# Performance work log

Hardware: AMD Instinct MI355X
Metric: run time of the kernel (lower is better)

The kernel has to match this reference:

```python
import jax, jax.numpy as jnp
import numpy as np

N_NODES = 100000


def gcn_conv(x, src, dst, W, b, n_nodes):
    # PyG GCNConv with self-loops already appended to (src, dst):
    # out_i = sum_{(j->i)} deg_j^{-1/2} deg_i^{-1/2} (x_j @ W) + b
    h = x @ W  # [N, out]
    deg = jnp.zeros((n_nodes,), dtype=x.dtype).at[dst].add(1.0)
    dinv = jnp.where(deg > 0, deg ** -0.5, 0.0)
    norm = dinv[src] * dinv[dst]  # [E']
    msg = h[src] * norm[:, None]  # gather + scale
    out = jax.ops.segment_sum(msg, dst, num_segments=n_nodes)
    return out + b


def setup_inputs() -> dict:
    key = jax.random.key(0)
    ks = jax.random.split(key, 12)
    N, E = N_NODES, 1600000
    C_IN, C_HID, C_OUT = 128, 128, 64
    x = jax.random.normal(ks[0], (N, C_IN), dtype=jnp.float32)
    edge_index = jax.random.randint(ks[1], (2, E), 0, N, dtype=jnp.int64)

    def lin(k, fan_in, fan_out):
        s = 1.0 / np.sqrt(fan_in)
        return jax.random.uniform(k, (fan_in, fan_out), minval=-s, maxval=s, dtype=jnp.float32)

    return {
        "x": x,
        "edge_index": edge_index,
        "W0": lin(ks[2], C_IN, C_HID), "b0": jnp.zeros((C_HID,), jnp.float32),
        "W1": lin(ks[3], C_HID, C_HID), "b1": jnp.zeros((C_HID,), jnp.float32),
        "W2": lin(ks[4], C_HID, C_OUT), "b2": jnp.zeros((C_OUT,), jnp.float32),
        "mlp_w1": lin(ks[5], C_OUT, 64),
        "mlp_b1": jax.random.uniform(ks[6], (64,), minval=-1/8, maxval=1/8, dtype=jnp.float32),
        "mlp_w2": lin(ks[7], 64, 2),
        "mlp_b2": jax.random.uniform(ks[8], (2,), minval=-1/8, maxval=1/8, dtype=jnp.float32),
    }


def reference(x, edge_index, W0, b0, W1, b1, W2, b2, mlp_w1, mlp_b1, mlp_w2, mlp_b2):
    N = x.shape[0]
    src0, dst0 = edge_index[0], edge_index[1]
    loop = jnp.arange(N, dtype=edge_index.dtype)
    src = jnp.concatenate([src0, loop])  # self-loops appended
    dst = jnp.concatenate([dst0, loop])

    h = jax.nn.relu(gcn_conv(x, src, dst, W0, b0, N))
    h = jax.nn.relu(gcn_conv(h, src, dst, W1, b1, N))
    h = gcn_conv(h, src, dst, W2, b2, N)  # [N, out]

    # edge feature = mean of endpoint node features (original edges only)
    ef = (h[src0] + h[dst0]) * 0.5  # [E, out]
    y = jax.nn.relu(ef @ mlp_w1 + mlp_b1) @ mlp_w2 + mlp_b2  # [E, 2]
    return y
```

## Files before the change

### kernel.cpp

```cpp
#include <hip/hip_runtime.h>


__device__ __forceinline__ int edge_at(const int* __restrict__ ei, long long idx, int is32) {
    return is32 ? ei[idx] : ei[2 * idx];
}

__device__ __forceinline__ unsigned short f2bf(float f) {
    unsigned int u = __float_as_uint(f);
    u += 0x7FFFu + ((u >> 16) & 1u);
    return (unsigned short)(u >> 16);
}
__device__ __forceinline__ float bf2f(unsigned short h) {
    return __uint_as_float(((unsigned int)h) << 16);
}

__global__ __launch_bounds__(256) void k_detect(const int4* __restrict__ ei4, int nchunks,
                                                int* __restrict__ flag) {
    int acc = 0;
    for (int i = blockIdx.x * 256 + threadIdx.x; i < nchunks; i += gridDim.x * 256) {
        int4 v = ei4[i];
        acc |= v.y | v.w;
    }
    if (__any(acc != 0)) {
        if ((threadIdx.x & 63) == 0) atomicOr(flag, 1);
    }
}

__global__ __launch_bounds__(256) void k_count(const int* __restrict__ ei, int E, int* __restrict__ cnt,
                                               int* __restrict__ rank, const int* __restrict__ flag) {
    int is32 = *flag;
    int e = blockIdx.x * 256 + threadIdx.x;
    if (e < E) {
        int d = edge_at(ei, (long long)E + e, is32);
        rank[e] = atomicAdd(&cnt[d], 1);
    }
}

__global__ __launch_bounds__(256) void k_scan_local(const int* __restrict__ cnt, int N,
                                                    int* __restrict__ offs, int* __restrict__ bsums) {
    __shared__ int wsum[4];
    int t = threadIdx.x;
    int lane = t & 63, wid = t >> 6;
    int gbase = blockIdx.x * 1024 + t * 4;
    int v0 = 0, v1 = 0, v2 = 0, v3 = 0;
    if (gbase + 0 < N) v0 = cnt[gbase + 0];
    if (gbase + 1 < N) v1 = cnt[gbase + 1];
    if (gbase + 2 < N) v2 = cnt[gbase + 2];
    if (gbase + 3 < N) v3 = cnt[gbase + 3];
    int tot = v0 + v1 + v2 + v3;
    int x = tot;
#pragma unroll
    for (int d = 1; d < 64; d <<= 1) {
        int y = __shfl_up(x, d);
        if (lane >= d) x += y;
    }
    if (lane == 63) wsum[wid] = x;
    __syncthreads();
    int wbase = 0;
#pragma unroll
    for (int w = 0; w < 4; w++)
        if (w < wid) wbase += wsum[w];
    int ex = wbase + x - tot;
    if (gbase + 0 < N) offs[gbase + 0] = ex;
    if (gbase + 1 < N) offs[gbase + 1] = ex + v0;
    if (gbase + 2 < N) offs[gbase + 2] = ex + v0 + v1;
    if (gbase + 3 < N) offs[gbase + 3] = ex + v0 + v1 + v2;
    if (t == 255) bsums[blockIdx.x] = wbase + x;
}

__global__ void k_scan_bsums(int* __restrict__ bsums, int nb) {
    int run = 0;
    for (int i = 0; i < nb; i++) {
        int v = bsums[i];
        bsums[i] = run;
        run += v;
    }
}

__global__ __launch_bounds__(256) void k_scan_add(int* __restrict__ offs, const int* __restrict__ bsums,
                                                  const int* __restrict__ cnt, float* __restrict__ dinv, int N) {
    int i = blockIdx.x * 256 + threadIdx.x;
    if (i < N) {
        offs[i] += bsums[i >> 10];
        dinv[i] = rsqrtf((float)(cnt[i] + 1));
    }
}

__global__ __launch_bounds__(256) void k_fill(const int* __restrict__ ei, int E,
                                              const int* __restrict__ offs, const int* __restrict__ rank,
                                              int* __restrict__ csr_src, const int* __restrict__ flag) {
    int is32 = *flag;
    int e = blockIdx.x * 256 + threadIdx.x;
    if (e < E) {
        int s = edge_at(ei, e, is32);
        int d = edge_at(ei, (long long)E + e, is32);
        int pos = offs[d] + rank[e];
        csr_src[pos] = s;
    }
}

template <int CIN, int COUT, bool RSCALE>
__global__ __launch_bounds__(256, 4) void k_gemm(const float* __restrict__ X, const float* __restrict__ W,
                                                 unsigned short* __restrict__ Y, int N,
                                                 const float* __restrict__ rscale) {
    constexpr int CT = COUT / 4;
    constexpr int RG = 256 / CT;
    constexpr int RPT = 64 / RG;
    constexpr int LDX = CIN + 4;
    __shared__ float xs[64 * LDX];
    int t = threadIdx.x;
    int r0 = blockIdx.x * 64;
    int nrows = (N - r0 < 64) ? (N - r0) : 64;
    for (int c = t; c < 64 * (CIN / 4); c += 256) {
        int row = c / (CIN / 4);
        int col = (c % (CIN / 4)) * 4;
        float4 v = make_float4(0.f, 0.f, 0.f, 0.f);
        if (row < nrows) v = *(const float4*)&X[(size_t)(r0 + row) * CIN + col];
        *(float4*)&xs[row * LDX + col] = v;
    }
    __syncthreads();

    int ct = t % CT, rg = t / CT;
    float4 acc[RPT];
#pragma unroll
    for (int j = 0; j < RPT; j++) acc[j] = make_float4(0.f, 0.f, 0.f, 0.f);
    const float* wp = W + ct * 4;
#pragma unroll 2
    for (int k = 0; k < CIN; k += 4) {
        float4 w0 = *(const float4*)&wp[(size_t)(k + 0) * COUT];
        float4 w1 = *(const float4*)&wp[(size_t)(k + 1) * COUT];
        float4 w2 = *(const float4*)&wp[(size_t)(k + 2) * COUT];
        float4 w3 = *(const float4*)&wp[(size_t)(k + 3) * COUT];
#pragma unroll
        for (int j = 0; j < RPT; j++) {
            float4 a = *(const float4*)&xs[(rg * RPT + j) * LDX + k];
            acc[j].x += a.x * w0.x + a.y * w1.x + a.z * w2.x + a.w * w3.x;
            acc[j].y += a.x * w0.y + a.y * w1.y + a.z * w2.y + a.w * w3.y;
            acc[j].z += a.x * w0.z + a.y * w1.z + a.z * w2.z + a.w * w3.z;
            acc[j].w += a.x * w0.w + a.y * w1.w + a.z * w2.w + a.w * w3.w;
        }
    }
#pragma unroll
    for (int j = 0; j < RPT; j++) {
        int row = r0 + rg * RPT + j;
        if (row < N) {
            float4 a = acc[j];
            if constexpr (RSCALE) {
                float s = rscale[row];
                a.x *= s; a.y *= s; a.z *= s; a.w *= s;
            }
            ushort4 o;
            o.x = f2bf(a.x); o.y = f2bf(a.y); o.z = f2bf(a.z); o.w = f2bf(a.w);
            *(ushort4*)&Y[(size_t)row * COUT + ct * 4] = o;
        }
    }
}

template <int C, bool RELU>
__global__ __launch_bounds__(256) void k_aggregate(const unsigned short* __restrict__ T,
                                                   const int* __restrict__ offs,
                                                   const int* __restrict__ cnt, const int* __restrict__ csr_src,
                                                   const float* __restrict__ dinv,
                                                   const float* __restrict__ bias, float* __restrict__ H, int N) {
    constexpr int LANES = C / 4;
    constexpr int NPB = 256 / LANES;
    int li = threadIdx.x & (LANES - 1);
    int g = threadIdx.x / LANES;
    int gw = blockIdx.x * NPB + g;
    if (gw >= N) return;
    int wl0 = (threadIdx.x & 63) - li;

    float4 acc = make_float4(0.f, 0.f, 0.f, 0.f);
    int num = cnt[gw];
    int start = offs[gw];
    for (int base = 0; base < num; base += LANES) {
        int sv = 0;
        if (base + li < num) sv = csr_src[start + base + li];
        int m = num - base;
        if (m > LANES) m = LANES;
        int j = 0;
        for (; j + 4 <= m; j += 4) {
            int s0 = __shfl(sv, wl0 + j + 0);
            int s1 = __shfl(sv, wl0 + j + 1);
            int s2 = __shfl(sv, wl0 + j + 2);
            int s3 = __shfl(sv, wl0 + j + 3);
            ushort4 a0 = *(const ushort4*)&T[(size_t)s0 * C + li * 4];
            ushort4 a1 = *(const ushort4*)&T[(size_t)s1 * C + li * 4];
            ushort4 a2 = *(const ushort4*)&T[(size_t)s2 * C + li * 4];
            ushort4 a3 = *(const ushort4*)&T[(size_t)s3 * C + li * 4];
            acc.x += bf2f(a0.x) + bf2f(a1.x) + bf2f(a2.x) + bf2f(a3.x);
            acc.y += bf2f(a0.y) + bf2f(a1.y) + bf2f(a2.y) + bf2f(a3.y);
            acc.z += bf2f(a0.z) + bf2f(a1.z) + bf2f(a2.z) + bf2f(a3.z);
            acc.w += bf2f(a0.w) + bf2f(a1.w) + bf2f(a2.w) + bf2f(a3.w);
        }
        for (; j < m; j++) {
            int s = __shfl(sv, wl0 + j);
            ushort4 a = *(const ushort4*)&T[(size_t)s * C + li * 4];
            acc.x += bf2f(a.x); acc.y += bf2f(a.y);
            acc.z += bf2f(a.z); acc.w += bf2f(a.w);
        }
    }
    float di = dinv[gw];
    ushort4 tsu = *(const ushort4*)&T[(size_t)gw * C + li * 4];
    float4 bb = *(const float4*)&bias[li * 4];
    float4 o;
    o.x = di * (acc.x + bf2f(tsu.x)) + bb.x;
    o.y = di * (acc.y + bf2f(tsu.y)) + bb.y;
    o.z = di * (acc.z + bf2f(tsu.z)) + bb.z;
    o.w = di * (acc.w + bf2f(tsu.w)) + bb.w;
    if (RELU) {
        o.x = fmaxf(o.x, 0.f); o.y = fmaxf(o.y, 0.f);
        o.z = fmaxf(o.z, 0.f); o.w = fmaxf(o.w, 0.f);
    }
    *(float4*)&H[(size_t)gw * C + li * 4] = o;
}

__global__ __launch_bounds__(256) void k_edge_mlp(const int* __restrict__ ei, int E,
                                                  const unsigned short* __restrict__ Z,
                                                  const float* __restrict__ b1,
                                                  const float* __restrict__ w2, const float* __restrict__ b2,
                                                  float* __restrict__ out, const int* __restrict__ flag) {
    int is32 = *flag;
    long long t = (long long)blockIdx.x * 256 + threadIdx.x;
    int e = (int)(t >> 4);
    int l = (int)(t & 15);
    if (e >= E) return;
    int s = edge_at(ei, e, is32);
    int d = edge_at(ei, (long long)E + e, is32);
    ushort4 zsu = *(const ushort4*)&Z[(size_t)s * 64 + l * 4];
    ushort4 zdu = *(const ushort4*)&Z[(size_t)d * 64 + l * 4];
    float4 bb = *(const float4*)&b1[l * 4];
    float4 u;
    u.x = fmaxf(0.f, 0.5f * (bf2f(zsu.x) + bf2f(zdu.x)) + bb.x);
    u.y = fmaxf(0.f, 0.5f * (bf2f(zsu.y) + bf2f(zdu.y)) + bb.y);
    u.z = fmaxf(0.f, 0.5f * (bf2f(zsu.z) + bf2f(zdu.z)) + bb.z);
    u.w = fmaxf(0.f, 0.5f * (bf2f(zsu.w) + bf2f(zdu.w)) + bb.w);
    float4 wa = *(const float4*)&w2[l * 8];
    float4 wb = *(const float4*)&w2[l * 8 + 4];
    float y0 = u.x * wa.x + u.y * wa.z + u.z * wb.x + u.w * wb.z;
    float y1 = u.x * wa.y + u.y * wa.w + u.z * wb.y + u.w * wb.w;
#pragma unroll
    for (int m = 1; m < 16; m <<= 1) {
        y0 += __shfl_xor(y0, m);
        y1 += __shfl_xor(y1, m);
    }
    if (l == 0) out[(size_t)e * 2 + 0] = y0 + b2[0];
    else if (l == 1) out[(size_t)e * 2 + 1] = y1 + b2[1];
}

extern "C" void kernel_launch(void* const* d_in, const int* in_sizes, int n_in,
                              void* d_out, int out_size, void* d_ws, size_t ws_size,
                              hipStream_t stream) {
    const float* x = (const float*)d_in[0];
    const int* ei = (const int*)d_in[1];
    const float* W0 = (const float*)d_in[2];
    const float* b0 = (const float*)d_in[3];
    const float* W1 = (const float*)d_in[4];
    const float* b1 = (const float*)d_in[5];
    const float* W2 = (const float*)d_in[6];
    const float* b2 = (const float*)d_in[7];
    const float* mw1 = (const float*)d_in[8];
    const float* mb1 = (const float*)d_in[9];
    const float* mw2 = (const float*)d_in[10];
    const float* mb2 = (const float*)d_in[11];
    float* out = (float*)d_out;

    int N = in_sizes[0] / 128;
    int E = in_sizes[1] / 2;

    char* p = (char*)d_ws;
    auto alloc = [&](size_t bytes) {
        char* q = p;
        p += (bytes + 255) & ~size_t(255);
        return q;
    };
    float* bufF = (float*)alloc((size_t)N * 128 * 4);
    unsigned short* bufH = (unsigned short*)alloc((size_t)N * 128 * 2);
    int* cnt = (int*)alloc((size_t)N * 4);
    int* offs = (int*)alloc((size_t)N * 4);
    float* dinv = (float*)alloc((size_t)N * 4);
    int* csr_src = (int*)alloc((size_t)E * 4);
    int* rank = (int*)alloc((size_t)E * 4);
    int* bsums = (int*)alloc(4096);
    int* flag = (int*)alloc(256);

    hipMemsetAsync(cnt, 0, (size_t)N * 4, stream);
    hipMemsetAsync(flag, 0, 4, stream);

    int gE = (E + 255) / 256;
    int gN = (N + 255) / 256;
    int nchunks = (2 * E) / 4;
    k_detect<<<1024, 256, 0, stream>>>((const int4*)ei, nchunks, flag);
    k_count<<<gE, 256, 0, stream>>>(ei, E, cnt, rank, flag);
    int nb = (N + 1023) / 1024;
    k_scan_local<<<nb, 256, 0, stream>>>(cnt, N, offs, bsums);
    k_scan_bsums<<<1, 1, 0, stream>>>(bsums, nb);
    k_scan_add<<<gN, 256, 0, stream>>>(offs, bsums, cnt, dinv, N);
    k_fill<<<gE, 256, 0, stream>>>(ei, E, offs, rank, csr_src, flag);

    int gG = (N + 63) / 64;
    int gA128 = (N + 7) / 8;
    int gA64 = (N + 15) / 16;

    k_gemm<128, 128, true><<<gG, 256, 0, stream>>>(x, W0, bufH, N, dinv);
    k_aggregate<128, true><<<gA128, 256, 0, stream>>>(bufH, offs, cnt, csr_src, dinv, b0, bufF, N);
    k_gemm<128, 128, true><<<gG, 256, 0, stream>>>(bufF, W1, bufH, N, dinv);
    k_aggregate<128, true><<<gA128, 256, 0, stream>>>(bufH, offs, cnt, csr_src, dinv, b1, bufF, N);
    k_gemm<128, 64, true><<<gG, 256, 0, stream>>>(bufF, W2, bufH, N, dinv);
    k_aggregate<64, false><<<gA64, 256, 0, stream>>>(bufH, offs, cnt, csr_src, dinv, b2, bufF, N);
    k_gemm<64, 64, false><<<gG, 256, 0, stream>>>(bufF, mw1, bufH, N, nullptr);

    long long totalT = (long long)E * 16;
    int gM = (int)((totalT + 255) / 256);
    k_edge_mlp<<<gM, 256, 0, stream>>>(ei, E, bufH, mb1, mw2, mb2, out, flag);
}
```

Measured before the change: 688.2 us.

## Split aggregation and edge MLP into column-chunk passes for cache locality

The 128-channel aggregation now runs as eight launches, each covering a 16-column slice (32 bytes per node row). The edge MLP runs as four passes over 16-column slices, accumulating the partial output in place. The aim is to shrink the working set of gathered feature rows so each pass fits in L2/LLC, turning random gathers into cache hits. The cost is rereading the CSR indices and edge lists many times, more launches, and extra read-modify-write traffic on the output.

```diff
diff --git a/kernel.cpp b/kernel.cpp
--- a/kernel.cpp
+++ b/kernel.cpp
@@ -1,5 +1,7 @@
 #include <hip/hip_runtime.h>
 
+
+typedef float f32x4 __attribute__((ext_vector_type(4)));
 
 __device__ __forceinline__ int edge_at(const int* __restrict__ ei, long long idx, int is32) {
     return is32 ? ei[idx] : ei[2 * idx];
@@ -154,6 +156,65 @@
             *(ushort4*)&Y[(size_t)row * COUT + ct * 4] = o;
         }
     }
+}
+
+template <bool RELU>
+__global__ __launch_bounds__(256) void k_agg16(const unsigned short* __restrict__ T,
+                                               const int* __restrict__ offs,
+                                               const int* __restrict__ cnt, const int* __restrict__ csr_src,
+                                               const float* __restrict__ dinv,
+                                               const float* __restrict__ bias, float* __restrict__ H,
+                                               int N, int ch) {
+    int li = threadIdx.x & 3;
+    int g = threadIdx.x >> 2;
+    int gw = blockIdx.x * 64 + g;
+    if (gw >= N) return;
+    int wl0 = (threadIdx.x & 63) - li;
+    int col = ch * 16 + li * 4;
+
+    float4 acc = make_float4(0.f, 0.f, 0.f, 0.f);
+    int num = cnt[gw];
+    int start = offs[gw];
+    int base = 0;
+    for (; base + 4 <= num; base += 4) {
+        int sv = __builtin_nontemporal_load(&csr_src[start + base + li]);
+        int s0 = __shfl(sv, wl0 + 0);
+        int s1 = __shfl(sv, wl0 + 1);
+        int s2 = __shfl(sv, wl0 + 2);
+        int s3 = __shfl(sv, wl0 + 3);
+        ushort4 a0 = *(const ushort4*)&T[(size_t)s0 * 128 + col];
+        ushort4 a1 = *(const ushort4*)&T[(size_t)s1 * 128 + col];
+        ushort4 a2 = *(const ushort4*)&T[(size_t)s2 * 128 + col];
+        ushort4 a3 = *(const ushort4*)&T[(size_t)s3 * 128 + col];
+        acc.x += bf2f(a0.x) + bf2f(a1.x) + bf2f(a2.x) + bf2f(a3.x);
+        acc.y += bf2f(a0.y) + bf2f(a1.y) + bf2f(a2.y) + bf2f(a3.y);
+        acc.z += bf2f(a0.z) + bf2f(a1.z) + bf2f(a2.z) + bf2f(a3.z);
+        acc.w += bf2f(a0.w) + bf2f(a1.w) + bf2f(a2.w) + bf2f(a3.w);
+    }
+    if (base < num) {
+        int sv = 0;
+        if (base + li < num) sv = __builtin_nontemporal_load(&csr_src[start + base + li]);
+        int m = num - base;
+        for (int j = 0; j < m; j++) {
+            int s = __shfl(sv, wl0 + j);
+            ushort4 a = *(const ushort4*)&T[(size_t)s * 128 + col];
+            acc.x += bf2f(a.x); acc.y += bf2f(a.y);
+            acc.z += bf2f(a.z); acc.w += bf2f(a.w);
+        }
+    }
+    float di = dinv[gw];
+    ushort4 ts = *(const ushort4*)&T[(size_t)gw * 128 + col];
+    float4 bb = *(const float4*)&bias[col];
+    f32x4 o;
+    o.x = di * (acc.x + bf2f(ts.x)) + bb.x;
+    o.y = di * (acc.y + bf2f(ts.y)) + bb.y;
+    o.z = di * (acc.z + bf2f(ts.z)) + bb.z;
+    o.w = di * (acc.w + bf2f(ts.w)) + bb.w;
+    if (RELU) {
+        o.x = fmaxf(o.x, 0.f); o.y = fmaxf(o.y, 0.f);
+        o.z = fmaxf(o.z, 0.f); o.w = fmaxf(o.w, 0.f);
+    }
+    __builtin_nontemporal_store(o, (f32x4*)&H[(size_t)gw * 128 + col]);
 }
 
 template <int C, bool RELU>
@@ -215,37 +276,45 @@
     *(float4*)&H[(size_t)gw * C + li * 4] = o;
 }
 
-__global__ __launch_bounds__(256) void k_edge_mlp(const int* __restrict__ ei, int E,
-                                                  const unsigned short* __restrict__ Z,
-                                                  const float* __restrict__ b1,
-                                                  const float* __restrict__ w2, const float* __restrict__ b2,
-                                                  float* __restrict__ out, const int* __restrict__ flag) {
+template <bool FIRST>
+__global__ __launch_bounds__(256) void k_emlp16(const int* __restrict__ ei, int E,
+                                                const unsigned short* __restrict__ Z,
+                                                const float* __restrict__ b1,
+                                                const float* __restrict__ w2, const float* __restrict__ b2,
+                                                float* __restrict__ out, const int* __restrict__ flag,
+                                                int ch) {
     int is32 = *flag;
     long long t = (long long)blockIdx.x * 256 + threadIdx.x;
-    int e = (int)(t >> 4);
-    int l = (int)(t & 15);
+    int e = (int)(t >> 2);
+    int li = (int)(t & 3);
     if (e >= E) return;
     int s = edge_at(ei, e, is32);
     int d = edge_at(ei, (long long)E + e, is32);
-    ushort4 zsu = *(const ushort4*)&Z[(size_t)s * 64 + l * 4];
-    ushort4 zdu = *(const ushort4*)&Z[(size_t)d * 64 + l * 4];
-    float4 bb = *(const float4*)&b1[l * 4];
+    int col = ch * 16 + li * 4;
+    ushort4 zsu = *(const ushort4*)&Z[(size_t)s * 64 + col];
+    ushort4 zdu = *(const ushort4*)&Z[(size_t)d * 64 + col];
+    float4 bb = *(const float4*)&b1[col];
     float4 u;
     u.x = fmaxf(0.f, 0.5f * (bf2f(zsu.x) + bf2f(zdu.x)) + bb.x);
     u.y = fmaxf(0.f, 0.5f * (bf2f(zsu.y) + bf2f(zdu.y)) + bb.y);
     u.z = fmaxf(0.f, 0.5f * (bf2f(zsu.z) + bf2f(zdu.z)) + bb.z);
     u.w = fmaxf(0.f, 0.5f * (bf2f(zsu.w) + bf2f(zdu.w)) + bb.w);
-    float4 wa = *(const float4*)&w2[l * 8];
-    float4 wb = *(const float4*)&w2[l * 8 + 4];
+    float4 wa = *(const float4*)&w2[col * 2];
+    float4 wb = *(const float4*)&w2[col * 2 + 4];
     float y0 = u.x * wa.x + u.y * wa.z + u.z * wb.x + u.w * wb.z;
     float y1 = u.x * wa.y + u.y * wa.w + u.z * wb.y + u.w * wb.w;
 #pragma unroll
-    for (int m = 1; m < 16; m <<= 1) {
+    for (int m = 1; m < 4; m <<= 1) {
         y0 += __shfl_xor(y0, m);
         y1 += __shfl_xor(y1, m);
     }
-    if (l == 0) out[(size_t)e * 2 + 0] = y0 + b2[0];
-    else if (l == 1) out[(size_t)e * 2 + 1] = y1 + b2[1];
+    if (FIRST) {
+        if (li == 0) out[(size_t)e * 2 + 0] = y0 + b2[0];
+        else if (li == 1) out[(size_t)e * 2 + 1] = y1 + b2[1];
+    } else {
+        if (li == 0) out[(size_t)e * 2 + 0] += y0;
+        else if (li == 1) out[(size_t)e * 2 + 1] += y1;
+    }
 }
 
 extern "C" void kernel_launch(void* const* d_in, const int* in_sizes, int n_in,
@@ -299,18 +368,22 @@
     k_fill<<<gE, 256, 0, stream>>>(ei, E, offs, rank, csr_src, flag);
 
     int gG = (N + 63) / 64;
-    int gA128 = (N + 7) / 8;
+    int gC = (N + 63) / 64;
     int gA64 = (N + 15) / 16;
 
     k_gemm<128, 128, true><<<gG, 256, 0, stream>>>(x, W0, bufH, N, dinv);
-    k_aggregate<128, true><<<gA128, 256, 0, stream>>>(bufH, offs, cnt, csr_src, dinv, b0, bufF, N);
+    for (int ch = 0; ch < 8; ch++)
+        k_agg16<true><<<gC, 256, 0, stream>>>(bufH, offs, cnt, csr_src, dinv, b0, bufF, N, ch);
     k_gemm<128, 128, true><<<gG, 256, 0, stream>>>(bufF, W1, bufH, N, dinv);
-    k_aggregate<128, true><<<gA128, 256, 0, stream>>>(bufH, offs, cnt, csr_src, dinv, b1, bufF, N);
+    for (int ch = 0; ch < 8; ch++)
+        k_agg16<true><<<gC, 256, 0, stream>>>(bufH, offs, cnt, csr_src, dinv, b1, bufF, N, ch);
     k_gemm<128, 64, true><<<gG, 256, 0, stream>>>(bufF, W2, bufH, N, dinv);
     k_aggregate<64, false><<<gA64, 256, 0, stream>>>(bufH, offs, cnt, csr_src, dinv, b2, bufF, N);
     k_gemm<64, 64, false><<<gG, 256, 0, stream>>>(bufF, mw1, bufH, N, nullptr);
 
-    long long totalT = (long long)E * 16;
+    long long totalT = (long long)E * 4;
     int gM = (int)((totalT + 255) / 256);
-    k_edge_mlp<<<gM, 256, 0, stream>>>(ei, E, bufH, mb1, mw2, mb2, out, flag);
-}
+    k_emlp16<true><<<gM, 256, 0, stream>>>(ei, E, bufH, mb1, mw2, mb2, out, flag, 0);
+    for (int ch = 1; ch < 4; ch++)
+        k_emlp16<false><<<gM, 256, 0, stream>>>(ei, E, bufH, mb1, mw2, mb2, out, flag, ch);
+}
```

Result: slower. 1.188 ms (+72.7%).

## Use bf16 MFMA for dense transforms and store aggregated activations in bf16

Applied to the files above, without the earlier changes.

Replaces the fp32 FMA GEMM with a bf16 MFMA 16x16x32 kernel that reads weights pre-packed into the MFMA operand layout by a new packing kernel. Aggregation outputs are now written as bf16, which halves intermediate activation traffic, and the next GEMM loads them directly. The cost is more bf16 rounding on the inputs and hidden activations, plus scalar 2-byte output stores from the MFMA kernel.

```diff
diff --git a/kernel.cpp b/kernel.cpp
--- a/kernel.cpp
+++ b/kernel.cpp
@@ -1,16 +1,20 @@
 #include <hip/hip_runtime.h>
 
+
+typedef unsigned short u16;
+typedef short bf16x8 __attribute__((ext_vector_type(8)));
+typedef float f32x4 __attribute__((ext_vector_type(4)));
 
 __device__ __forceinline__ int edge_at(const int* __restrict__ ei, long long idx, int is32) {
     return is32 ? ei[idx] : ei[2 * idx];
 }
 
-__device__ __forceinline__ unsigned short f2bf(float f) {
+__device__ __forceinline__ u16 f2bf(float f) {
     unsigned int u = __float_as_uint(f);
     u += 0x7FFFu + ((u >> 16) & 1u);
-    return (unsigned short)(u >> 16);
-}
-__device__ __forceinline__ float bf2f(unsigned short h) {
+    return (u16)(u >> 16);
+}
+__device__ __forceinline__ float bf2f(u16 h) {
     return __uint_as_float(((unsigned int)h) << 16);
 }
 
@@ -99,69 +103,97 @@
     }
 }
 
-template <int CIN, int COUT, bool RSCALE>
-__global__ __launch_bounds__(256, 4) void k_gemm(const float* __restrict__ X, const float* __restrict__ W,
-                                                 unsigned short* __restrict__ Y, int N,
-                                                 const float* __restrict__ rscale) {
-    constexpr int CT = COUT / 4;
-    constexpr int RG = 256 / CT;
-    constexpr int RPT = 64 / RG;
-    constexpr int LDX = CIN + 4;
-    __shared__ float xs[64 * LDX];
+template <int CIN, int COUT>
+__global__ __launch_bounds__(256) void k_packW(const float* __restrict__ W, u16* __restrict__ P) {
+    constexpr int KS = CIN / 32;
+    int idx = blockIdx.x * 256 + threadIdx.x;
+    int total = (COUT / 16) * KS * 64;
+    if (idx >= total) return;
+    int l = idx & 63;
+    int t = idx >> 6;
+    int ks = t % KS, ct = t / KS;
+    int c = ct * 16 + (l & 15);
+    int k0 = ks * 32 + (l >> 4) * 8;
+    u16 o[8];
+#pragma unroll
+    for (int j = 0; j < 8; j++) o[j] = f2bf(W[(size_t)(k0 + j) * COUT + c]);
+    *(ushort4*)&P[(size_t)idx * 8 + 0] = make_ushort4(o[0], o[1], o[2], o[3]);
+    *(ushort4*)&P[(size_t)idx * 8 + 4] = make_ushort4(o[4], o[5], o[6], o[7]);
+}
+
+template <int CIN, int COUT, bool RSCALE, bool AFP32>
+__global__ __launch_bounds__(256) void k_gemm_mfma(const void* __restrict__ Xv,
+                                                   const u16* __restrict__ Wp,
+                                                   u16* __restrict__ Y, int N,
+                                                   const float* __restrict__ rscale) {
+    constexpr int KS = CIN / 32;
+    constexpr int CT = COUT / 16;
+    constexpr int LDA = CIN + 8;
+    __shared__ u16 As[64 * LDA];
     int t = threadIdx.x;
     int r0 = blockIdx.x * 64;
-    int nrows = (N - r0 < 64) ? (N - r0) : 64;
-    for (int c = t; c < 64 * (CIN / 4); c += 256) {
-        int row = c / (CIN / 4);
-        int col = (c % (CIN / 4)) * 4;
-        float4 v = make_float4(0.f, 0.f, 0.f, 0.f);
-        if (row < nrows) v = *(const float4*)&X[(size_t)(r0 + row) * CIN + col];
-        *(float4*)&xs[row * LDX + col] = v;
+
+    if (AFP32) {
+        const float* X = (const float*)Xv;
+        for (int i = t * 4; i < 64 * CIN; i += 1024) {
+            int row = i / CIN, col = i % CIN;
+            float4 v = make_float4(0.f, 0.f, 0.f, 0.f);
+            int grow = r0 + row;
+            if (grow < N) v = *(const float4*)&X[(size_t)grow * CIN + col];
+            *(ushort4*)&As[row * LDA + col] = make_ushort4(f2bf(v.x), f2bf(v.y), f2bf(v.z), f2bf(v.w));
+        }
+    } else {
+        const u16* X = (const u16*)Xv;
+        for (int i = t * 8; i < 64 * CIN; i += 2048) {
+            int row = i / CIN, col = i % CIN;
+            uint4 v = make_uint4(0, 0, 0, 0);
+            int grow = r0 + row;
+            if (grow < N) v = *(const uint4*)&X[(size_t)grow * CIN + col];
+            *(uint4*)&As[row * LDA + col] = v;
+        }
     }
     __syncthreads();
 
-    int ct = t % CT, rg = t / CT;
-    float4 acc[RPT];
-#pragma unroll
-    for (int j = 0; j < RPT; j++) acc[j] = make_float4(0.f, 0.f, 0.f, 0.f);
-    const float* wp = W + ct * 4;
-#pragma unroll 2
-    for (int k = 0; k < CIN; k += 4) {
-        float4 w0 = *(const float4*)&wp[(size_t)(k + 0) * COUT];
-        float4 w1 = *(const float4*)&wp[(size_t)(k + 1) * COUT];
-        float4 w2 = *(const float4*)&wp[(size_t)(k + 2) * COUT];
-        float4 w3 = *(const float4*)&wp[(size_t)(k + 3) * COUT];
-#pragma unroll
-        for (int j = 0; j < RPT; j++) {
-            float4 a = *(const float4*)&xs[(rg * RPT + j) * LDX + k];
-            acc[j].x += a.x * w0.x + a.y * w1.x + a.z * w2.x + a.w * w3.x;
-            acc[j].y += a.x * w0.y + a.y * w1.y + a.z * w2.y + a.w * w3.y;
-            acc[j].z += a.x * w0.z + a.y * w1.z + a.z * w2.z + a.w * w3.z;
-            acc[j].w += a.x * w0.w + a.y * w1.w + a.z * w2.w + a.w * w3.w;
-        }
-    }
-#pragma unroll
-    for (int j = 0; j < RPT; j++) {
-        int row = r0 + rg * RPT + j;
-        if (row < N) {
-            float4 a = acc[j];
-            if constexpr (RSCALE) {
-                float s = rscale[row];
-                a.x *= s; a.y *= s; a.z *= s; a.w *= s;
+    int w = t >> 6;
+    int l = t & 63;
+    int lr = l & 15;
+    int lk = l >> 4;
+    f32x4 acc[CT];
+#pragma unroll
+    for (int i = 0; i < CT; i++) {
+        f32x4 z = {0.f, 0.f, 0.f, 0.f};
+        acc[i] = z;
+    }
+    const u16* arow = &As[(w * 16 + lr) * LDA + lk * 8];
+#pragma unroll
+    for (int ks = 0; ks < KS; ks++) {
+        bf16x8 a = *(const bf16x8*)&arow[ks * 32];
+#pragma unroll
+        for (int ct = 0; ct < CT; ct++) {
+            bf16x8 b = *(const bf16x8*)&Wp[((size_t)(ct * KS + ks) * 64 + l) * 8];
+            acc[ct] = __builtin_amdgcn_mfma_f32_16x16x32_bf16(a, b, acc[ct], 0, 0, 0);
+        }
+    }
+#pragma unroll
+    for (int i = 0; i < 4; i++) {
+        int grow = r0 + w * 16 + lk * 4 + i;
+        if (grow < N) {
+            float s = 1.f;
+            if (RSCALE) s = rscale[grow];
+#pragma unroll
+            for (int ct = 0; ct < CT; ct++) {
+                Y[(size_t)grow * COUT + ct * 16 + lr] = f2bf(acc[ct][i] * s);
             }
-            ushort4 o;
-            o.x = f2bf(a.x); o.y = f2bf(a.y); o.z = f2bf(a.z); o.w = f2bf(a.w);
-            *(ushort4*)&Y[(size_t)row * COUT + ct * 4] = o;
         }
     }
 }
 
 template <int C, bool RELU>
-__global__ __launch_bounds__(256) void k_aggregate(const unsigned short* __restrict__ T,
+__global__ __launch_bounds__(256) void k_aggregate(const u16* __restrict__ T,
                                                    const int* __restrict__ offs,
                                                    const int* __restrict__ cnt, const int* __restrict__ csr_src,
                                                    const float* __restrict__ dinv,
-                                                   const float* __restrict__ bias, float* __restrict__ H, int N) {
+                                                   const float* __restrict__ bias, u16* __restrict__ H, int N) {
     constexpr int LANES = C / 4;
     constexpr int NPB = 256 / LANES;
     int li = threadIdx.x & (LANES - 1);
@@ -203,20 +235,19 @@
     float di = dinv[gw];
     ushort4 tsu = *(const ushort4*)&T[(size_t)gw * C + li * 4];
     float4 bb = *(const float4*)&bias[li * 4];
-    float4 o;
-    o.x = di * (acc.x + bf2f(tsu.x)) + bb.x;
-    o.y = di * (acc.y + bf2f(tsu.y)) + bb.y;
-    o.z = di * (acc.z + bf2f(tsu.z)) + bb.z;
-    o.w = di * (acc.w + bf2f(tsu.w)) + bb.w;
+    float ox = di * (acc.x + bf2f(tsu.x)) + bb.x;
+    float oy = di * (acc.y + bf2f(tsu.y)) + bb.y;
+    float oz = di * (acc.z + bf2f(tsu.z)) + bb.z;
+    float ow = di * (acc.w + bf2f(tsu.w)) + bb.w;
     if (RELU) {
-        o.x = fmaxf(o.x, 0.f); o.y = fmaxf(o.y, 0.f);
-        o.z = fmaxf(o.z, 0.f); o.w = fmaxf(o.w, 0.f);
-    }
-    *(float4*)&H[(size_t)gw * C + li * 4] = o;
+        ox = fmaxf(ox, 0.f); oy = fmaxf(oy, 0.f);
+        oz = fmaxf(oz, 0.f); ow = fmaxf(ow, 0.f);
+    }
+    *(ushort4*)&H[(size_t)gw * C + li * 4] = make_ushort4(f2bf(ox), f2bf(oy), f2bf(oz), f2bf(ow));
 }
 
 __global__ __launch_bounds__(256) void k_edge_mlp(const int* __restrict__ ei, int E,
-                                                  const unsigned short* __restrict__ Z,
+                                                  const u16* __restrict__ Z,
                                                   const float* __restrict__ b1,
                                                   const float* __restrict__ w2, const float* __restrict__ b2,
                                                   float* __restrict__ out, const int* __restrict__ flag) {
@@ -274,8 +305,8 @@
         p += (bytes + 255) & ~size_t(255);
         return q;
     };
-    float* bufF = (float*)alloc((size_t)N * 128 * 4);
-    unsigned short* bufH = (unsigned short*)alloc((size_t)N * 128 * 2);
+    u16* bufA = (u16*)alloc((size_t)N * 128 * 2);
+    u16* bufB = (u16*)alloc((size_t)N * 128 * 2);
     int* cnt = (int*)alloc((size_t)N * 4);
     int* offs = (int*)alloc((size_t)N * 4);
     float* dinv = (float*)alloc((size_t)N * 4);
@@ -283,6 +314,10 @@
     int* rank = (int*)alloc((size_t)E * 4);
     int* bsums = (int*)alloc(4096);
     int* flag = (int*)alloc(256);
+    u16* pW0 = (u16*)alloc(128 * 128 * 2);
+    u16* pW1 = (u16*)alloc(128 * 128 * 2);
+    u16* pW2 = (u16*)alloc(128 * 64 * 2);
+    u16* pZ = (u16*)alloc(64 * 64 * 2);
 
     hipMemsetAsync(cnt, 0, (size_t)N * 4, stream);
     hipMemsetAsync(flag, 0, 4, stream);
@@ -291,6 +326,10 @@
     int gN = (N + 255) / 256;
     int nchunks = (2 * E) / 4;
     k_detect<<<1024, 256, 0, stream>>>((const int4*)ei, nchunks, flag);
+    k_packW<128, 128><<<8, 256, 0, stream>>>(W0, pW0);
+    k_packW<128, 128><<<8, 256, 0, stream>>>(W1, pW1);
+    k_packW<128, 64><<<4, 256, 0, stream>>>(W2, pW2);
+    k_packW<64, 64><<<2, 256, 0, stream>>>(mw1, pZ);
     k_count<<<gE, 256, 0, stream>>>(ei, E, cnt, rank, flag);
     int nb = (N + 1023) / 1024;
     k_scan_local<<<nb, 256, 0, stream>>>(cnt, N, offs, bsums);
@@ -302,15 +341,15 @@
     int gA128 = (N + 7) / 8;
     int gA64 = (N + 15) / 16;
 
-    k_gemm<128, 128, true><<<gG, 256, 0, stream>>>(x, W0, bufH, N, dinv);
-    k_aggregate<128, true><<<gA128, 256, 0, stream>>>(bufH, offs, cnt, csr_src, dinv, b0, bufF, N);
-    k_gemm<128, 128, true><<<gG, 256, 0, stream>>>(bufF, W1, bufH, N, dinv);
-    k_aggregate<128, true><<<gA128, 256, 0, stream>>>(bufH, offs, cnt, csr_src, dinv, b1, bufF, N);
-    k_gemm<128, 64, true><<<gG, 256, 0, stream>>>(bufF, W2, bufH, N, dinv);
-    k_aggregate<64, false><<<gA64, 256, 0, stream>>>(bufH, offs, cnt, csr_src, dinv, b2, bufF, N);
-    k_gemm<64, 64, false><<<gG, 256, 0, stream>>>(bufF, mw1, bufH, N, nullptr);
+    k_gemm_mfma<128, 128, true, true><<<gG, 256, 0, stream>>>(x, pW0, bufA, N, dinv);
+    k_aggregate<128, true><<<gA128, 256, 0, stream>>>(bufA, offs, cnt, csr_src, dinv, b0, bufB, N);
+    k_gemm_mfma<128, 128, true, false><<<gG, 256, 0, stream>>>(bufB, pW1, bufA, N, dinv);
+    k_aggregate<128, true><<<gA128, 256, 0, stream>>>(bufA, offs, cnt, csr_src, dinv, b1, bufB, N);
+    k_gemm_mfma<128, 64, true, false><<<gG, 256, 0, stream>>>(bufB, pW2, bufA, N, dinv);
+    k_aggregate<64, false><<<gA64, 256, 0, stream>>>(bufA, offs, cnt, csr_src, dinv, b2, bufB, N);
+    k_gemm_mfma<64, 64, false, false><<<gG, 256, 0, stream>>>(bufB, pZ, bufA, N, nullptr);
 
     long long totalT = (long long)E * 16;
     int gM = (int)((totalT + 255) / 256);
-    k_edge_mlp<<<gM, 256, 0, stream>>>(ei, E, bufH, mb1, mw2, mb2, out, flag);
-}
+    k_edge_mlp<<<gM, 256, 0, stream>>>(ei, E, bufA, mb1, mw2, mb2, out, flag);
+}
```

New measurement: 574.5 us. 16.5% less time.
